# Kernel tuning notes

Measured on AMD Instinct MI355X. Metric: run time of the kernel, lower is better.

Reference implementation:

```python
import jax, jax.numpy as jnp
import numpy as np

DIM = 768
NUM_HEADS = 12
HEAD_DIM = DIM // NUM_HEADS


def setup_inputs() -> dict:
    key = jax.random.key(0)
    k0, k1, k2 = jax.random.split(key, 3)
    B, N = 8, 1024
    x = jax.random.normal(k0, (B, N, DIM), dtype=jnp.float32)
    w_qkv = jax.random.normal(k1, (DIM, 3 * DIM), dtype=jnp.float32) * (DIM ** -0.5)
    b_qkv = jnp.zeros((3 * DIM,), dtype=jnp.float32)
    w_proj = jax.random.normal(k2, (DIM, DIM), dtype=jnp.float32) * (DIM ** -0.5)
    b_proj = jnp.zeros((DIM,), dtype=jnp.float32)
    return {"x": x, "w_qkv": w_qkv, "b_qkv": b_qkv, "w_proj": w_proj, "b_proj": b_proj}


def reference(x, w_qkv, b_qkv, w_proj, b_proj):
    B, N, C = x.shape
    scale = HEAD_DIM ** -0.5
    qkv = x @ w_qkv + b_qkv                                  # [B, N, 3*C]
    qkv = qkv.reshape(B, N, 3, NUM_HEADS, HEAD_DIM).transpose(2, 0, 3, 1, 4)
    q, k, v = qkv[0], qkv[1], qkv[2]                          # each [B, H, N, hd]
    attn = jnp.einsum('bhqd,bhkd->bhqk', q, k) * scale        # [B, H, N, N]
    attn = jax.nn.softmax(attn, axis=-1)
    out = jnp.einsum('bhqk,bhkd->bhqd', attn, v)              # [B, H, N, hd]
    out = out.transpose(0, 2, 1, 3).reshape(B, N, C)
    return out @ w_proj + b_proj
```

## Files before the change

### kernel.cpp

```cpp
#include <hip/hip_runtime.h>
#include <cstdint>
#include <cmath>

#define B_ 8
#define S_ 1024
#define D_ 768
#define H_ 12
#define HD_ 64

typedef __bf16 bf16;
typedef __attribute__((ext_vector_type(8))) __bf16 bf16x8;
typedef __attribute__((ext_vector_type(4))) float floatx4;

typedef const __attribute__((address_space(1))) unsigned int* gas_ptr;
typedef __attribute__((address_space(3))) unsigned int* las_ptr;

__device__ __forceinline__ void async_ld16(const void* g, void* l) {
    gas_ptr gp = (gas_ptr)(uintptr_t)g;
    las_ptr lp = (las_ptr)(unsigned)(uintptr_t)l;
    __builtin_amdgcn_global_load_lds(gp, lp, 16, 0, 0);
}

__device__ __forceinline__ void xcd_swizzle(int& bx, int& by) {
    const int nx = gridDim.x, ny = gridDim.y;
    const int lin = blockIdx.y * nx + blockIdx.x;
    const int xcd = lin & 7;
    const int loc = lin >> 3;
    by = xcd * (ny >> 3) + loc / nx;
    bx = loc % nx;
}

__device__ __forceinline__ void transpose_dev(const float* __restrict__ in,
                                              bf16* __restrict__ out,
                                              int N, int K, int n0, int k0,
                                              bf16 (*tile)[66], int tid) {
#pragma unroll
    for (int r = 0; r < 4; r++) {
        int idx = r * 256 + tid;
        int row = idx >> 4;
        int c0  = (idx & 15) * 4;
        float4 v = *(const float4*)(in + (size_t)(k0 + row) * N + n0 + c0);
        tile[c0 + 0][row] = (bf16)v.x;
        tile[c0 + 1][row] = (bf16)v.y;
        tile[c0 + 2][row] = (bf16)v.z;
        tile[c0 + 3][row] = (bf16)v.w;
    }
    __syncthreads();
#pragma unroll
    for (int r = 0; r < 2; r++) {
        int idx = r * 256 + tid;
        int orow = idx >> 3;
        int kk   = (idx & 7) * 8;
        union { bf16x8 v; bf16 e[8]; } u;
#pragma unroll
        for (int j = 0; j < 8; j++) u.e[j] = tile[orow][kk + j];
        *(bf16x8*)(out + (size_t)(n0 + orow) * K + k0 + kk) = u.v;
    }
}

__global__ __launch_bounds__(256) void prep_all(
    const float* __restrict__ x, const float* __restrict__ w_qkv,
    const float* __restrict__ w_proj,
    bf16* __restrict__ xb, bf16* __restrict__ wqkvt, bf16* __restrict__ wprojt)
{
    __shared__ bf16 tile[64][66];
    const int blk = blockIdx.x, tid = threadIdx.x;
    if (blk < 6144) {
        int i = (blk * 256 + tid) * 4;
        float4 v = *(const float4*)(x + i);
        xb[i]     = (bf16)v.x;
        xb[i + 1] = (bf16)v.y;
        xb[i + 2] = (bf16)v.z;
        xb[i + 3] = (bf16)v.w;
    } else if (blk < 6576) {
        int t = blk - 6144;
        transpose_dev(w_qkv, wqkvt, 2304, 768, (t % 36) * 64, (t / 36) * 64, tile, tid);
    } else {
        int t = blk - 6576;
        transpose_dev(w_proj, wprojt, 768, 768, (t % 12) * 64, (t / 12) * 64, tile, tid);
    }
}

__global__ void transpose_v(const bf16* __restrict__ vbuf, bf16* __restrict__ vt) {
    __shared__ bf16 tile[64][66];
    const int tid = threadIdx.x;
    const int kt = blockIdx.x, h = blockIdx.y, b = blockIdx.z;
    const bf16* src = vbuf + ((size_t)b * S_ + (size_t)kt * 64) * D_ + h * 64;
#pragma unroll
    for (int r = 0; r < 2; r++) {
        int idx = r * 256 + tid;
        int kr = idx >> 3;
        int d0 = (idx & 7) * 8;
        bf16x8 v = *(const bf16x8*)(src + (size_t)kr * D_ + d0);
#pragma unroll
        for (int j = 0; j < 8; j++) {
            int p  = d0 + j;
            int dt = (p >> 2) + 16 * (p & 3);
            tile[dt][kr] = v[j];
        }
    }
    __syncthreads();
    bf16* dst = vt + ((size_t)(b * H_ + h) * 64) * 1024 + kt * 64;
#pragma unroll
    for (int r = 0; r < 2; r++) {
        int idx = r * 256 + tid;
        int dr = idx >> 3;
        int k0 = (idx & 7) * 8;
        union { bf16x8 v; bf16 e[8]; } u;
#pragma unroll
        for (int j = 0; j < 8; j++) {
            int kp  = k0 + j;
            int grp = kp & 32;
            int w32 = kp & 31;
            int gg  = w32 >> 3;
            int jj  = w32 & 7;
            int tk  = grp + ((jj < 4) ? (4 * gg + jj) : (16 + 4 * gg + jj - 4));
            u.e[j] = tile[dr][tk];
        }
        *(bf16x8*)(dst + (size_t)dr * 1024 + k0) = u.v;
    }
}

__global__ __launch_bounds__(256, 3) void gemm_qkv(
    const bf16* __restrict__ A, const bf16* __restrict__ Bt,
    const float* __restrict__ bias,
    bf16* __restrict__ qpack, bf16* __restrict__ kpack, bf16* __restrict__ vbuf)
{
    __shared__ __align__(16) bf16 As[2][128 * 32];
    __shared__ __align__(16) bf16 Bs[2][128 * 32];
    const int N = 2304, K = 768;

    const int tid  = threadIdx.x;
    const int lane = tid & 63;
    const int w    = tid >> 6;
    const int wm   = (w >> 1) * 64;
    const int wn   = (w & 1) * 64;
    int bx, by;
    xcd_swizzle(bx, by);
    const long m0  = (long)by * 128;
    const long n0  = (long)bx * 128;
    const int c    = lane & 15;
    const int g    = lane >> 4;

    const floatx4 fzero = {0.f, 0.f, 0.f, 0.f};
    floatx4 acc[4][4];
#pragma unroll
    for (int i = 0; i < 4; i++)
#pragma unroll
        for (int j = 0; j < 4; j++) acc[i][j] = fzero;

    for (int k0 = 0; k0 < K; k0 += 64) {
        __syncthreads();
#pragma unroll
        for (int s = 0; s < 2; s++) {
            const int kb = k0 + s * 32;
#pragma unroll
            for (int r = 0; r < 2; r++) {
                const int idx = r * 256 + tid;
                const int rr  = idx >> 2;
                const int kc  = (idx & 3) * 8;
                async_ld16(A  + (m0 + rr) * (long)K + kb + kc, (char*)As[s] + idx * 16);
                async_ld16(Bt + (n0 + rr) * (long)K + kb + kc, (char*)Bs[s] + idx * 16);
            }
        }
        __syncthreads();

#pragma unroll
        for (int s = 0; s < 2; s++) {
            bf16x8 af[4], bfr[4];
#pragma unroll
            for (int i = 0; i < 4; i++) {
                af[i]  = *(const bf16x8*)(As[s] + (wm + i * 16 + c) * 32 + g * 8);
                bfr[i] = *(const bf16x8*)(Bs[s] + (wn + i * 16 + c) * 32 + g * 8);
            }
#pragma unroll
            for (int i = 0; i < 4; i++)
#pragma unroll
                for (int j = 0; j < 4; j++)
                    acc[i][j] = __builtin_amdgcn_mfma_f32_16x16x32_bf16(af[i], bfr[j], acc[i][j], 0, 0, 0);
        }
    }

    const int head = (int)((n0 + wn) >> 6);
    const int rm   = wm + g * 4;
    float bv[4];
#pragma unroll
    for (int j = 0; j < 4; j++) bv[j] = bias[(int)n0 + wn + c + 16 * j];
    const int bb    = (int)(m0 >> 10);
    const int sbase = ((int)m0 & 1023) + rm;

    if (head < 24) {
        const float sc = (head < 12) ? 0.125f : 1.0f;
        bf16* dst = ((head < 12) ? qpack : kpack)
                  + (((size_t)((bb * H_ + (head < 12 ? head : head - 12)) * 1024 + sbase)) << 6)
                  + 4 * c;
#pragma unroll
        for (int i = 0; i < 4; i++)
#pragma unroll
            for (int e = 0; e < 4; e++) {
                union { bf16 h4[4]; uint64_t u; } pk;
#pragma unroll
                for (int j = 0; j < 4; j++) pk.h4[j] = (bf16)((acc[i][j][e] + bv[j]) * sc);
                *(uint64_t*)(dst + (size_t)(i * 16 + e) * 64) = pk.u;
            }
    } else {
        bf16* dst = vbuf + ((size_t)(bb * 1024 + sbase)) * 768 + (head - 24) * 64 + 4 * c;
#pragma unroll
        for (int i = 0; i < 4; i++)
#pragma unroll
            for (int e = 0; e < 4; e++) {
                union { bf16 h4[4]; uint64_t u; } pk;
#pragma unroll
                for (int j = 0; j < 4; j++) pk.h4[j] = (bf16)(acc[i][j][e] + bv[j]);
                *(uint64_t*)(dst + (size_t)(i * 16 + e) * 768) = pk.u;
            }
    }
}

__global__ __launch_bounds__(256, 3) void gemm_bt(
    const bf16* __restrict__ A, const bf16* __restrict__ Bt,
    const float* __restrict__ bias, float* __restrict__ C,
    int M, int N, int K)
{
    __shared__ __align__(16) bf16 As[2][128 * 32];
    __shared__ __align__(16) bf16 Bs[2][128 * 32];

    const int tid  = threadIdx.x;
    const int lane = tid & 63;
    const int w    = tid >> 6;
    const int wm   = (w >> 1) * 64;
    const int wn   = (w & 1) * 64;
    int bx, by;
    xcd_swizzle(bx, by);
    const long m0  = (long)by * 128;
    const long n0  = (long)bx * 128;
    const int c    = lane & 15;
    const int g    = lane >> 4;

    const floatx4 fzero = {0.f, 0.f, 0.f, 0.f};
    floatx4 acc[4][4];
#pragma unroll
    for (int i = 0; i < 4; i++)
#pragma unroll
        for (int j = 0; j < 4; j++) acc[i][j] = fzero;

    for (int k0 = 0; k0 < K; k0 += 64) {
        __syncthreads();
#pragma unroll
        for (int s = 0; s < 2; s++) {
            const int kb = k0 + s * 32;
#pragma unroll
            for (int r = 0; r < 2; r++) {
                const int idx = r * 256 + tid;
                const int rr  = idx >> 2;
                const int kc  = (idx & 3) * 8;
                async_ld16(A  + (m0 + rr) * (long)K + kb + kc, (char*)As[s] + idx * 16);
                async_ld16(Bt + (n0 + rr) * (long)K + kb + kc, (char*)Bs[s] + idx * 16);
            }
        }
        __syncthreads();

#pragma unroll
        for (int s = 0; s < 2; s++) {
            bf16x8 af[4], bfr[4];
#pragma unroll
            for (int i = 0; i < 4; i++) {
                af[i]  = *(const bf16x8*)(As[s] + (wm + i * 16 + c) * 32 + g * 8);
                bfr[i] = *(const bf16x8*)(Bs[s] + (wn + i * 16 + c) * 32 + g * 8);
            }
#pragma unroll
            for (int i = 0; i < 4; i++)
#pragma unroll
                for (int j = 0; j < 4; j++)
                    acc[i][j] = __builtin_amdgcn_mfma_f32_16x16x32_bf16(af[i], bfr[j], acc[i][j], 0, 0, 0);
        }
    }

    const int cn = wn + c;
    const int rm = wm + g * 4;
#pragma unroll
    for (int j = 0; j < 4; j++) {
        const long gn = n0 + cn + j * 16;
        const float bv = bias[gn];
#pragma unroll
        for (int i = 0; i < 4; i++) {
            const long gm = m0 + rm + i * 16;
#pragma unroll
            for (int e = 0; e < 4; e++)
                C[(gm + e) * (long)N + gn] = acc[i][j][e] + bv;
        }
    }
}

__global__ __launch_bounds__(128, 3) void attn_fused(
    const bf16* __restrict__ qpack, const bf16* __restrict__ kpack,
    const bf16* __restrict__ vt, bf16* __restrict__ outp)
{
    __shared__ __align__(16) bf16 Ks[2048];
    __shared__ __align__(16) bf16 Vs[2048];

    const int tid  = threadIdx.x;
    const int lane = tid & 63;
    const int w    = tid >> 6;
    const int g    = lane >> 4;
    const int c    = lane & 15;

    const int id = blockIdx.x;
    const int bh = id % 96;
    const int qt = id / 96;
    const int h  = bh >> 3;
    const int b  = bh & 7;
    const int q0 = qt * 64 + w * 32;
    const bf16* qpb = qpack + ((size_t)(b * H_ + h) * 1024) * 64;
    const bf16* kpb = kpack + ((size_t)(b * H_ + h) * 1024) * 64;
    const bf16* vtb = vt    + ((size_t)(b * H_ + h) * 64) * 1024;

    bf16x8 qf[2][2];
#pragma unroll
    for (int qb = 0; qb < 2; qb++)
#pragma unroll
        for (int dc = 0; dc < 2; dc++)
            qf[qb][dc] = *(const bf16x8*)(qpb + (size_t)(q0 + qb * 16 + c) * 64 + dc * 32 + g * 8);

    union { uint32_t u[4]; bf16x8 v; } onesu;
    onesu.u[0] = onesu.u[1] = onesu.u[2] = onesu.u[3] = 0x3F803F80u;
    const bf16x8 onesf = onesu.v;

    const floatx4 fzero = {0.f, 0.f, 0.f, 0.f};
    floatx4 oacc[2][4];
    floatx4 lacc[2];
#pragma unroll
    for (int qb = 0; qb < 2; qb++) {
        lacc[qb] = fzero;
#pragma unroll
        for (int db = 0; db < 4; db++) oacc[qb][db] = fzero;
    }

    for (int kt = 0; kt < 32; kt++) {
        const int kg = kt * 32;
        __syncthreads();
#pragma unroll
        for (int r = 0; r < 2; r++) {
            const int i  = r * 128 + tid;
            const int dc = i >> 7, key = (i >> 2) & 31, dch = i & 3;
            async_ld16(kpb + (size_t)(kg + key) * 64 + dc * 32 + dch * 8, (char*)Ks + i * 16);
        }
#pragma unroll
        for (int r = 0; r < 2; r++) {
            const int i = r * 128 + tid;
            const int d = i >> 2, kch = i & 3;
            async_ld16(vtb + (size_t)d * 1024 + kg + kch * 8, (char*)Vs + i * 16);
        }
        __syncthreads();

        bf16x8 kf[2][2];
#pragma unroll
        for (int kb = 0; kb < 2; kb++)
#pragma unroll
            for (int dc = 0; dc < 2; dc++)
                kf[kb][dc] = *(const bf16x8*)(Ks + (dc * 32 + kb * 16 + c) * 32 + g * 8);

        bf16x8 vf[4];
#pragma unroll
        for (int db = 0; db < 4; db++)
            vf[db] = *(const bf16x8*)(Vs + (db * 16 + c) * 32 + g * 8);

#pragma unroll
        for (int qb = 0; qb < 2; qb++) {
            floatx4 s0 = fzero, s1 = fzero;
#pragma unroll
            for (int dc = 0; dc < 2; dc++) {
                s0 = __builtin_amdgcn_mfma_f32_16x16x32_bf16(kf[0][dc], qf[qb][dc], s0, 0, 0, 0);
                s1 = __builtin_amdgcn_mfma_f32_16x16x32_bf16(kf[1][dc], qf[qb][dc], s1, 0, 0, 0);
            }
            union { bf16 e[8]; bf16x8 v; } pa;
#pragma unroll
            for (int e4 = 0; e4 < 4; e4++) {
                pa.e[e4]     = (bf16)__expf(s0[e4]);
                pa.e[e4 + 4] = (bf16)__expf(s1[e4]);
            }
            lacc[qb] = __builtin_amdgcn_mfma_f32_16x16x32_bf16(onesf, pa.v, lacc[qb], 0, 0, 0);
#pragma unroll
            for (int db = 0; db < 4; db++)
                oacc[qb][db] = __builtin_amdgcn_mfma_f32_16x16x32_bf16(vf[db], pa.v, oacc[qb][db], 0, 0, 0);
        }
    }

#pragma unroll
    for (int qb = 0; qb < 2; qb++) {
        const float linv = 1.0f / lacc[qb][0];
        bf16* orow = outp + ((size_t)b * S_ + q0 + qb * 16 + c) * D_ + h * 64;
#pragma unroll
        for (int db = 0; db < 4; db++)
#pragma unroll
            for (int f = 0; f < 2; f++) {
                union { bf16 hh[2]; uint32_t u; } pk_;
                pk_.hh[0] = (bf16)(oacc[qb][db][2 * f]     * linv);
                pk_.hh[1] = (bf16)(oacc[qb][db][2 * f + 1] * linv);
                *(uint32_t*)(orow + db * 16 + 4 * g + 2 * f) = pk_.u;
            }
    }
}

extern "C" void kernel_launch(void* const* d_in, const int* in_sizes, int n_in,
                              void* d_out, int out_size, void* d_ws, size_t ws_size,
                              hipStream_t stream) {
    const float* x      = (const float*)d_in[0];
    const float* w_qkv  = (const float*)d_in[1];
    const float* b_qkv  = (const float*)d_in[2];
    const float* w_proj = (const float*)d_in[3];
    const float* b_proj = (const float*)d_in[4];
    float* out = (float*)d_out;

    bf16* xb     = (bf16*)d_ws;
    bf16* wqkvt  = xb     + (size_t)8192 * 768;
    bf16* wprojt = wqkvt  + (size_t)2304 * 768;
    bf16* qpack  = wprojt + (size_t)768 * 768;
    bf16* kpack  = qpack  + (size_t)96 * 1024 * 64;
    bf16* vbuf   = kpack  + (size_t)96 * 1024 * 64;
    bf16* vt     = vbuf   + (size_t)8192 * 768;
    bf16* attnb  = xb;

    prep_all<<<6720, 256, 0, stream>>>(x, w_qkv, w_proj, xb, wqkvt, wprojt);
    gemm_qkv<<<dim3(18, 64), 256, 0, stream>>>(xb, wqkvt, b_qkv, qpack, kpack, vbuf);
    transpose_v<<<dim3(16, 12, 8), 256, 0, stream>>>(vbuf, vt);
    attn_fused<<<1536, 128, 0, stream>>>(qpack, kpack, vt, attnb);
    gemm_bt<<<dim3(6, 64), 256, 0, stream>>>(attnb, wprojt, b_proj, out, 8192, 768, 768);
}
```

Baseline: 189.3 us.

## Software-pipeline GEMM K-loop with double-buffered async LDS prefetch

Both GEMM kernels previously loaded two 32-wide K slices, waited, then computed with no overlap between loads and MFMA. They now prefetch the next 32-wide slice into the alternate LDS buffer while computing on the current one, with one barrier per step. Launch bounds also drop from 3 to 2 blocks per SM, which gives more registers but lowers occupancy. The barrier count per K element stays the same, and the overlap depends on async loads being in flight during the MFMA work.

```diff
diff --git a/kernel.cpp b/kernel.cpp
--- a/kernel.cpp
+++ b/kernel.cpp
@@ -28,6 +28,20 @@
     const int loc = lin >> 3;
     by = xcd * (ny >> 3) + loc / nx;
     bx = loc % nx;
+}
+
+__device__ __forceinline__ void stage32(const bf16* __restrict__ A,
+                                        const bf16* __restrict__ Bt,
+                                        long m0, long n0, long K, int kb,
+                                        bf16* Asb, bf16* Bsb, int tid) {
+#pragma unroll
+    for (int r = 0; r < 2; r++) {
+        const int idx = r * 256 + tid;
+        const int rr  = idx >> 2;
+        const int kc  = (idx & 3) * 8;
+        async_ld16(A  + (m0 + rr) * K + kb + kc, (char*)Asb + idx * 16);
+        async_ld16(Bt + (n0 + rr) * K + kb + kc, (char*)Bsb + idx * 16);
+    }
 }
 
 __device__ __forceinline__ void transpose_dev(const float* __restrict__ in,
@@ -121,7 +135,7 @@
     }
 }
 
-__global__ __launch_bounds__(256, 3) void gemm_qkv(
+__global__ __launch_bounds__(256, 2) void gemm_qkv(
     const bf16* __restrict__ A, const bf16* __restrict__ Bt,
     const float* __restrict__ bias,
     bf16* __restrict__ qpack, bf16* __restrict__ kpack, bf16* __restrict__ vbuf)
@@ -129,6 +143,7 @@
     __shared__ __align__(16) bf16 As[2][128 * 32];
     __shared__ __align__(16) bf16 Bs[2][128 * 32];
     const int N = 2304, K = 768;
+    const int NKT = K / 32;
 
     const int tid  = threadIdx.x;
     const int lane = tid & 63;
@@ -149,36 +164,27 @@
 #pragma unroll
         for (int j = 0; j < 4; j++) acc[i][j] = fzero;
 
-    for (int k0 = 0; k0 < K; k0 += 64) {
+    stage32(A, Bt, m0, n0, K, 0, As[0], Bs[0], tid);
+    __syncthreads();
+
+    for (int kt = 0; kt < NKT; kt++) {
+        const int cur = kt & 1;
+        if (kt + 1 < NKT)
+            stage32(A, Bt, m0, n0, K, (kt + 1) * 32, As[cur ^ 1], Bs[cur ^ 1], tid);
+
+        bf16x8 af[4], bfr[4];
+#pragma unroll
+        for (int i = 0; i < 4; i++) {
+            af[i]  = *(const bf16x8*)(As[cur] + (wm + i * 16 + c) * 32 + g * 8);
+            bfr[i] = *(const bf16x8*)(Bs[cur] + (wn + i * 16 + c) * 32 + g * 8);
+        }
+#pragma unroll
+        for (int i = 0; i < 4; i++)
+#pragma unroll
+            for (int j = 0; j < 4; j++)
+                acc[i][j] = __builtin_amdgcn_mfma_f32_16x16x32_bf16(af[i], bfr[j], acc[i][j], 0, 0, 0);
+
         __syncthreads();
-#pragma unroll
-        for (int s = 0; s < 2; s++) {
-            const int kb = k0 + s * 32;
-#pragma unroll
-            for (int r = 0; r < 2; r++) {
-                const int idx = r * 256 + tid;
-                const int rr  = idx >> 2;
-                const int kc  = (idx & 3) * 8;
-                async_ld16(A  + (m0 + rr) * (long)K + kb + kc, (char*)As[s] + idx * 16);
-                async_ld16(Bt + (n0 + rr) * (long)K + kb + kc, (char*)Bs[s] + idx * 16);
-            }
-        }
-        __syncthreads();
-
-#pragma unroll
-        for (int s = 0; s < 2; s++) {
-            bf16x8 af[4], bfr[4];
-#pragma unroll
-            for (int i = 0; i < 4; i++) {
-                af[i]  = *(const bf16x8*)(As[s] + (wm + i * 16 + c) * 32 + g * 8);
-                bfr[i] = *(const bf16x8*)(Bs[s] + (wn + i * 16 + c) * 32 + g * 8);
-            }
-#pragma unroll
-            for (int i = 0; i < 4; i++)
-#pragma unroll
-                for (int j = 0; j < 4; j++)
-                    acc[i][j] = __builtin_amdgcn_mfma_f32_16x16x32_bf16(af[i], bfr[j], acc[i][j], 0, 0, 0);
-        }
     }
 
     const int head = (int)((n0 + wn) >> 6);
@@ -217,7 +223,7 @@
     }
 }
 
-__global__ __launch_bounds__(256, 3) void gemm_bt(
+__global__ __launch_bounds__(256, 2) void gemm_bt(
     const bf16* __restrict__ A, const bf16* __restrict__ Bt,
     const float* __restrict__ bias, float* __restrict__ C,
     int M, int N, int K)
@@ -236,6 +242,7 @@
     const long n0  = (long)bx * 128;
     const int c    = lane & 15;
     const int g    = lane >> 4;
+    const int NKT  = K / 32;
 
     const floatx4 fzero = {0.f, 0.f, 0.f, 0.f};
     floatx4 acc[4][4];
@@ -244,36 +251,27 @@
 #pragma unroll
         for (int j = 0; j < 4; j++) acc[i][j] = fzero;
 
-    for (int k0 = 0; k0 < K; k0 += 64) {
+    stage32(A, Bt, m0, n0, K, 0, As[0], Bs[0], tid);
+    __syncthreads();
+
+    for (int kt = 0; kt < NKT; kt++) {
+        const int cur = kt & 1;
+        if (kt + 1 < NKT)
+            stage32(A, Bt, m0, n0, K, (kt + 1) * 32, As[cur ^ 1], Bs[cur ^ 1], tid);
+
+        bf16x8 af[4], bfr[4];
+#pragma unroll
+        for (int i = 0; i < 4; i++) {
+            af[i]  = *(const bf16x8*)(As[cur] + (wm + i * 16 + c) * 32 + g * 8);
+            bfr[i] = *(const bf16x8*)(Bs[cur] + (wn + i * 16 + c) * 32 + g * 8);
+        }
+#pragma unroll
+        for (int i = 0; i < 4; i++)
+#pragma unroll
+            for (int j = 0; j < 4; j++)
+                acc[i][j] = __builtin_amdgcn_mfma_f32_16x16x32_bf16(af[i], bfr[j], acc[i][j], 0, 0, 0);
+
         __syncthreads();
-#pragma unroll
-        for (int s = 0; s < 2; s++) {
-            const int kb = k0 + s * 32;
-#pragma unroll
-            for (int r = 0; r < 2; r++) {
-                const int idx = r * 256 + tid;
-                const int rr  = idx >> 2;
-                const int kc  = (idx & 3) * 8;
-                async_ld16(A  + (m0 + rr) * (long)K + kb + kc, (char*)As[s] + idx * 16);
-                async_ld16(Bt + (n0 + rr) * (long)K + kb + kc, (char*)Bs[s] + idx * 16);
-            }
-        }
-        __syncthreads();
-
-#pragma unroll
-        for (int s = 0; s < 2; s++) {
-            bf16x8 af[4], bfr[4];
-#pragma unroll
-            for (int i = 0; i < 4; i++) {
-                af[i]  = *(const bf16x8*)(As[s] + (wm + i * 16 + c) * 32 + g * 8);
-                bfr[i] = *(const bf16x8*)(Bs[s] + (wn + i * 16 + c) * 32 + g * 8);
-            }
-#pragma unroll
-            for (int i = 0; i < 4; i++)
-#pragma unroll
-                for (int j = 0; j < 4; j++)
-                    acc[i][j] = __builtin_amdgcn_mfma_f32_16x16x32_bf16(af[i], bfr[j], acc[i][j], 0, 0, 0);
-        }
     }
 
     const int cn = wn + c;
```

Result: no change. 190.8 us (+0.8%).
